# Performance work log

Hardware: AMD Instinct MI355X
Metric: run time of the kernel (lower is better)

The kernel has to match this reference:

```python
import jax, jax.numpy as jnp
import numpy as np


def setup_inputs() -> dict:
    key = jax.random.key(0)
    k1, k2, k3 = jax.random.split(key, 3)
    B, S, E = 4, 4096, 512
    x = jax.random.normal(k1, (B, S, E), dtype=jnp.float32)
    # xavier_uniform for Linear weights; zero biases (per _reset_parameters)
    lim_qkv = float(np.sqrt(6.0 / (E + 3 * E)))
    W_qkv = jax.random.uniform(k2, (3 * E, E), minval=-lim_qkv, maxval=lim_qkv, dtype=jnp.float32)
    b_qkv = jnp.zeros((3 * E,), dtype=jnp.float32)
    lim_out = float(np.sqrt(6.0 / (E + E)))
    W_out = jax.random.uniform(k3, (E, E), minval=-lim_out, maxval=lim_out, dtype=jnp.float32)
    b_out = jnp.zeros((E,), dtype=jnp.float32)
    return {"x": x, "W_qkv": W_qkv, "b_qkv": b_qkv, "W_out": W_out, "b_out": b_out}


def reference(x, W_qkv, b_qkv, W_out, b_out):
    B, S, E = x.shape
    H = 8
    D = E // H
    qkv = x @ W_qkv.T + b_qkv                      # [B,S,3E]
    qkv = qkv.reshape(B, S, H, 3 * D)
    q, k, v = jnp.split(qkv, 3, axis=-1)            # each [B,S,H,D]
    q = jax.nn.sigmoid(q)
    k = jax.nn.sigmoid(k)
    # flow conservation normalizers (sum over seq dim=1, then feature dim=3)
    i = jnp.sum(q * jnp.sum(k, axis=1, keepdims=True), axis=3, keepdims=True)      # [B,S,H,1]
    o = jnp.sum(k * jnp.sum(q, axis=1, keepdims=True), axis=3, keepdims=True)
    i_hat = jnp.sum(q * jnp.sum(k / o, axis=1, keepdims=True), axis=3, keepdims=True)
    o_hat = jnp.sum(k * jnp.sum(q / i, axis=1, keepdims=True), axis=3, keepdims=True)
    # NOTE: faithful to source — matmul batches over (B,S) and contracts the HEAD axis
    vw = v * jax.nn.softmax(o_hat, axis=1)          # [B,S,H,D]
    kv = jnp.einsum('bshd,bshe->bsde', k, vw)       # [B,S,D,D]
    r = jnp.einsum('bshd,bsde->bshe', q / i, kv) * jax.nn.sigmoid(i_hat)  # [B,S,H,D]
    values = r.reshape(B, S, E)
    return values @ W_out.T + b_out
```

## Files before the change

### kernel.cpp

```cpp
#include <hip/hip_runtime.h>
#include <cstdint>
#include <cstddef>

#define B_ 4
#define S_ 4096
#define E_ 512
#define NPOS 16384
#define QKVC 1536
#define K_ 512

typedef unsigned short u16;
typedef u16    u16x8  __attribute__((ext_vector_type(8)));
typedef u16    u16x4  __attribute__((ext_vector_type(4)));
typedef __bf16 bf16x8 __attribute__((ext_vector_type(8)));
typedef float  f32x4  __attribute__((ext_vector_type(4)));

__device__ __forceinline__ u16 f2bf(float f) {
    unsigned u = __builtin_bit_cast(unsigned, f);
    unsigned r = (u + 0x7fffu + ((u >> 16) & 1u)) >> 16;
    return (u16)r;
}
__device__ __forceinline__ float bf2f(u16 u) {
    return __builtin_bit_cast(float, (unsigned)u << 16);
}
__device__ __forceinline__ float rcpf(float x) { return __builtin_amdgcn_rcpf(x); }

__device__ __forceinline__ void async16(const void* g, void* lds) {
    __builtin_amdgcn_global_load_lds(
        (const __attribute__((address_space(1))) unsigned int*)g,
        (__attribute__((address_space(3))) unsigned int*)lds, 16, 0, 0);
}

__global__ void cvt_kernel(const float4* __restrict__ in, u16x4* __restrict__ out, int n4) {
    int i = blockIdx.x * 256 + threadIdx.x;
    if (i < n4) {
        float4 v = in[i];
        u16x4 o;
        o[0] = f2bf(v.x); o[1] = f2bf(v.y); o[2] = f2bf(v.z); o[3] = f2bf(v.w);
        out[i] = o;
    }
}

__global__ __launch_bounds__(256) void gemm_qkv(
        const u16* __restrict__ A, const u16* __restrict__ Bw,
        const float* __restrict__ bias,
        u16* __restrict__ Qb, u16* __restrict__ Kb, u16* __restrict__ Vb,
        int K) {
    __shared__ u16 As[128 * 32];
    __shared__ u16 Bs[128 * 32];
    const int tid  = threadIdx.x;
    const int wave = tid >> 6, lane = tid & 63;
    const int m0 = blockIdx.y * 128, n0 = blockIdx.x * 128;
    const int wm = (wave & 1) * 64, wn = (wave >> 1) * 64;

    const int srow = wave * 16 + (lane >> 2);
    const int scol = (lane & 3) * 8;
    const u16* Ap = A  + (size_t)(m0 + srow) * K + scol;
    const u16* Bp = Bw + (size_t)(n0 + srow) * K + scol;
    u16* AsW = &As[wave * 512];
    u16* BsW = &Bs[wave * 512];
    const size_t rstep = (size_t)64 * K;

    f32x4 acc[4][4] = {};
    const int fr = lane & 15, fk = (lane >> 4) * 8;

    for (int k0 = 0; k0 < K; k0 += 32) {
        async16(Ap + k0,         AsW);
        async16(Ap + k0 + rstep, AsW + 2048);
        async16(Bp + k0,         BsW);
        async16(Bp + k0 + rstep, BsW + 2048);
        __syncthreads();
        bf16x8 a[4], b[4];
        #pragma unroll
        for (int i = 0; i < 4; ++i)
            a[i] = *(const bf16x8*)&As[(wm + i * 16 + fr) * 32 + fk];
        #pragma unroll
        for (int j = 0; j < 4; ++j)
            b[j] = *(const bf16x8*)&Bs[(wn + j * 16 + fr) * 32 + fk];
        #pragma unroll
        for (int i = 0; i < 4; ++i)
            #pragma unroll
            for (int j = 0; j < 4; ++j)
                acc[i][j] = __builtin_amdgcn_mfma_f32_16x16x32_bf16(a[i], b[j], acc[i][j], 0, 0, 0);
        __syncthreads();
    }

    const int cn = lane & 15, rb = (lane >> 4) * 4;
    const int cg   = (n0 + wn) >> 6;
    const int type = cg % 3;
    const int hb   = cg / 3;
    u16* dst = (type == 0) ? Qb : (type == 1) ? Kb : Vb;
    const bool sg = (type < 2);
    #pragma unroll
    for (int i = 0; i < 4; ++i) {
        int mbase = m0 + wm + i * 16 + rb;
        #pragma unroll
        for (int j = 0; j < 4; ++j) {
            int ccol = j * 16 + cn;
            float bv = bias[n0 + wn + ccol];
            int outcol = hb * 64 + ccol;
            f32x4 av = acc[i][j];
            #pragma unroll
            for (int r = 0; r < 4; ++r) {
                float v = av[r] + bv;
                if (sg) v = 1.f / (1.f + __expf(-v));
                dst[(size_t)(mbase + r) * 512 + outcol] = f2bf(v);
            }
        }
    }
}

__global__ __launch_bounds__(256) void gemm_out(
        const u16* __restrict__ A, const u16* __restrict__ Bw,
        const float* __restrict__ bias, float* __restrict__ C,
        int N, int K) {
    __shared__ u16 As[128 * 32];
    __shared__ u16 Bs[128 * 32];
    const int tid  = threadIdx.x;
    const int wave = tid >> 6, lane = tid & 63;
    const int m0 = blockIdx.y * 128, n0 = blockIdx.x * 128;
    const int wm = (wave & 1) * 64, wn = (wave >> 1) * 64;
    const int srow = wave * 16 + (lane >> 2);
    const int scol = (lane & 3) * 8;
    const u16* Ap = A  + (size_t)(m0 + srow) * K + scol;
    const u16* Bp = Bw + (size_t)(n0 + srow) * K + scol;
    u16* AsW = &As[wave * 512];
    u16* BsW = &Bs[wave * 512];
    const size_t rstep = (size_t)64 * K;
    f32x4 acc[4][4] = {};
    const int fr = lane & 15, fk = (lane >> 4) * 8;
    for (int k0 = 0; k0 < K; k0 += 32) {
        async16(Ap + k0,         AsW);
        async16(Ap + k0 + rstep, AsW + 2048);
        async16(Bp + k0,         BsW);
        async16(Bp + k0 + rstep, BsW + 2048);
        __syncthreads();
        bf16x8 a[4], b[4];
        #pragma unroll
        for (int i = 0; i < 4; ++i)
            a[i] = *(const bf16x8*)&As[(wm + i * 16 + fr) * 32 + fk];
        #pragma unroll
        for (int j = 0; j < 4; ++j)
            b[j] = *(const bf16x8*)&Bs[(wn + j * 16 + fr) * 32 + fk];
        #pragma unroll
        for (int i = 0; i < 4; ++i)
            #pragma unroll
            for (int j = 0; j < 4; ++j)
                acc[i][j] = __builtin_amdgcn_mfma_f32_16x16x32_bf16(a[i], b[j], acc[i][j], 0, 0, 0);
        __syncthreads();
    }
    const int cn = lane & 15, rb = (lane >> 4) * 4;
    #pragma unroll
    for (int i = 0; i < 4; ++i) {
        int mbase = m0 + wm + i * 16 + rb;
        #pragma unroll
        for (int j = 0; j < 4; ++j) {
            int nn = n0 + wn + j * 16 + cn;
            float bv = bias[nn];
            f32x4 av = acc[i][j];
            #pragma unroll
            for (int r = 0; r < 4; ++r)
                C[(size_t)(mbase + r) * N + nn] = av[r] + bv;
        }
    }
}

__global__ __launch_bounds__(256) void sum_qk(const u16* __restrict__ Qg, const u16* __restrict__ Kg,
                                              float* __restrict__ sumq, float* __restrict__ sumk) {
    int b = blockIdx.x, sc = blockIdx.y;
    int w = threadIdx.x >> 6, lane = threadIdx.x & 63;
    float aq[8] = {}, ak[8] = {};
    int p0 = b * S_ + sc * 32 + w * 8;
    for (int it = 0; it < 8; ++it) {
        size_t off = (size_t)(p0 + it) * 512 + lane * 8;
        u16x8 q8 = *(const u16x8*)(Qg + off);
        u16x8 k8 = *(const u16x8*)(Kg + off);
        #pragma unroll
        for (int j = 0; j < 8; ++j) { aq[j] += bf2f(q8[j]); ak[j] += bf2f(k8[j]); }
    }
    __shared__ float red[4][1024];
    #pragma unroll
    for (int j = 0; j < 8; ++j) {
        red[w][lane * 8 + j]       = aq[j];
        red[w][512 + lane * 8 + j] = ak[j];
    }
    __syncthreads();
    int t = threadIdx.x;
    #pragma unroll
    for (int rr = 0; rr < 4; ++rr) {
        int slot = rr * 256 + t;
        float s = red[0][slot] + red[1][slot] + red[2][slot] + red[3][slot];
        float* dst = (slot < 512) ? &sumq[b * 512 + slot] : &sumk[b * 512 + (slot - 512)];
        atomicAdd(dst, s);
    }
}

__global__ __launch_bounds__(256) void fused_io(const u16* __restrict__ Qg, const u16* __restrict__ Kg,
                                                const float* __restrict__ sumq, const float* __restrict__ sumk,
                                                float* __restrict__ iv,
                                                float* __restrict__ sumqi, float* __restrict__ sumko) {
    int b = blockIdx.x, sc = blockIdx.y;
    int w = threadIdx.x >> 6, lane = threadIdx.x & 63;
    float skL[8], sqL[8];
    #pragma unroll
    for (int j = 0; j < 8; ++j) {
        skL[j] = sumk[b * 512 + lane * 8 + j];
        sqL[j] = sumq[b * 512 + lane * 8 + j];
    }
    float aqi[8] = {}, ako[8] = {};
    int p0 = b * S_ + sc * 32 + w * 8;
    for (int it = 0; it < 8; ++it) {
        int p = p0 + it;
        size_t off = (size_t)p * 512 + lane * 8;
        u16x8 q8 = *(const u16x8*)(Qg + off);
        u16x8 k8 = *(const u16x8*)(Kg + off);
        float qf[8], kf[8];
        #pragma unroll
        for (int j = 0; j < 8; ++j) { qf[j] = bf2f(q8[j]); kf[j] = bf2f(k8[j]); }
        float di = 0.f, dox = 0.f;
        #pragma unroll
        for (int j = 0; j < 8; ++j) { di += qf[j] * skL[j]; dox += kf[j] * sqL[j]; }
        di  += __shfl_xor(di, 1);  di  += __shfl_xor(di, 2);  di  += __shfl_xor(di, 4);
        dox += __shfl_xor(dox, 1); dox += __shfl_xor(dox, 2); dox += __shfl_xor(dox, 4);
        if ((lane & 7) == 0) iv[(size_t)p * 8 + (lane >> 3)] = di;
        float ri = rcpf(di), ro = rcpf(dox);
        #pragma unroll
        for (int j = 0; j < 8; ++j) { aqi[j] += qf[j] * ri; ako[j] += kf[j] * ro; }
    }
    __shared__ float red[4][1024];
    #pragma unroll
    for (int j = 0; j < 8; ++j) {
        red[w][lane * 8 + j]       = aqi[j];
        red[w][512 + lane * 8 + j] = ako[j];
    }
    __syncthreads();
    int t = threadIdx.x;
    #pragma unroll
    for (int rr = 0; rr < 4; ++rr) {
        int slot = rr * 256 + t;
        float s = red[0][slot] + red[1][slot] + red[2][slot] + red[3][slot];
        float* dst = (slot < 512) ? &sumqi[b * 512 + slot] : &sumko[b * 512 + (slot - 512)];
        atomicAdd(dst, s);
    }
}

__global__ __launch_bounds__(256) void io2_kernel(const u16* __restrict__ Qg, const u16* __restrict__ Kg,
                                                  const float* __restrict__ sumqi, const float* __restrict__ sumko,
                                                  const float* __restrict__ iv,
                                                  float* __restrict__ rowsc, float* __restrict__ wexp,
                                                  float* __restrict__ sm) {
    int b = blockIdx.x, sc = blockIdx.y;
    int w = threadIdx.x >> 6, lane = threadIdx.x & 63;
    float skoL[8], sqiL[8];
    #pragma unroll
    for (int j = 0; j < 8; ++j) {
        skoL[j] = sumko[b * 512 + lane * 8 + j];
        sqiL[j] = sumqi[b * 512 + lane * 8 + j];
    }
    float smacc = 0.f;
    int p0 = b * S_ + sc * 32 + w * 8;
    for (int it = 0; it < 8; ++it) {
        int p = p0 + it;
        size_t off = (size_t)p * 512 + lane * 8;
        u16x8 q8 = *(const u16x8*)(Qg + off);
        u16x8 k8 = *(const u16x8*)(Kg + off);
        float dih = 0.f, doh = 0.f;
        #pragma unroll
        for (int j = 0; j < 8; ++j) {
            dih += bf2f(q8[j]) * skoL[j];
            doh += bf2f(k8[j]) * sqiL[j];
        }
        dih += __shfl_xor(dih, 1); dih += __shfl_xor(dih, 2); dih += __shfl_xor(dih, 4);
        doh += __shfl_xor(doh, 1); doh += __shfl_xor(doh, 2); doh += __shfl_xor(doh, 4);
        if ((lane & 7) == 0) {
            int h = lane >> 3;
            float sig = 1.f / (1.f + __expf(-dih));
            rowsc[(size_t)p * 8 + h] = sig * rcpf(iv[(size_t)p * 8 + h]);
            float we = __expf(fminf(doh, 80.f));
            wexp[(size_t)p * 8 + h] = we;
            smacc += we;
        }
    }
    __shared__ float sr[4][8];
    if ((lane & 7) == 0) sr[w][lane >> 3] = smacc;
    __syncthreads();
    if (threadIdx.x < 8)
        atomicAdd(&sm[b * 8 + threadIdx.x],
                  sr[0][threadIdx.x] + sr[1][threadIdx.x] + sr[2][threadIdx.x] + sr[3][threadIdx.x]);
}

__global__ __launch_bounds__(256) void finalize_kernel(
        const u16* __restrict__ Qg, const u16* __restrict__ Kg, const u16* __restrict__ Vg,
        const float* __restrict__ rowsc, const float* __restrict__ wexp, const float* __restrict__ sm,
        u16* __restrict__ Rg) {
    __shared__ float Ml[4][2][8][9];
    __shared__ float vw[4][2][8][68];
    int w = threadIdx.x >> 6, lane = threadIdx.x & 63;
    int p0 = (blockIdx.x * 4 + w) * 2;
    int b = p0 >> 12;

    {
        int pl = (lane >> 3) & 1, hh = lane & 7, quad = lane >> 4;
        const u16* qa = Qg + (size_t)(p0 + pl) * 512 + hh * 64 + quad * 8;
        const u16* ka = Kg + (size_t)(p0 + pl) * 512 + hh * 64 + quad * 8;
        bf16x8 a0 = __builtin_bit_cast(bf16x8, *(const u16x8*)qa);
        bf16x8 a1 = __builtin_bit_cast(bf16x8, *(const u16x8*)(qa + 32));
        bf16x8 b0 = __builtin_bit_cast(bf16x8, *(const u16x8*)ka);
        bf16x8 b1 = __builtin_bit_cast(bf16x8, *(const u16x8*)(ka + 32));
        f32x4 accm = {0.f, 0.f, 0.f, 0.f};
        accm = __builtin_amdgcn_mfma_f32_16x16x32_bf16(a0, b0, accm, 0, 0, 0);
        accm = __builtin_amdgcn_mfma_f32_16x16x32_bf16(a1, b1, accm, 0, 0, 0);
        if (((lane >> 5) & 1) == ((lane >> 3) & 1)) {
            int plm = lane >> 5, hr = ((lane >> 4) & 1) * 4, h2 = lane & 7;
            #pragma unroll
            for (int r = 0; r < 4; ++r) Ml[w][plm][hr + r][h2] = accm[r];
        }
    }
    {
        int hv = lane >> 3, e0 = (lane & 7) * 8;
        float invsm = rcpf(sm[b * 8 + hv]);
        #pragma unroll
        for (int pl = 0; pl < 2; ++pl) {
            u16x8 v8 = *(const u16x8*)(Vg + (size_t)(p0 + pl) * 512 + lane * 8);
            float wgt = wexp[(size_t)(p0 + pl) * 8 + hv] * invsm;
            f32x4 x0, x1;
            #pragma unroll
            for (int j = 0; j < 4; ++j) { x0[j] = bf2f(v8[j]) * wgt; x1[j] = bf2f(v8[4 + j]) * wgt; }
            *(f32x4*)&vw[w][pl][hv][e0]     = x0;
            *(f32x4*)&vw[w][pl][hv][e0 + 4] = x1;
        }
    }
    __syncthreads();
    {
        int pl = lane >> 5, idx = lane & 31, h = idx >> 2, eq = (idx & 3) * 16;
        float out[16] = {};
        #pragma unroll
        for (int h2 = 0; h2 < 8; ++h2) {
            float m = Ml[w][pl][h][h2];
            #pragma unroll
            for (int c = 0; c < 4; ++c) {
                f32x4 vv = *(const f32x4*)&vw[w][pl][h2][eq + c * 4];
                #pragma unroll
                for (int j = 0; j < 4; ++j) out[c * 4 + j] += m * vv[j];
            }
        }
        float rs = rowsc[(size_t)(p0 + pl) * 8 + h];
        u16x8 o0, o1;
        #pragma unroll
        for (int j = 0; j < 8; ++j) { o0[j] = f2bf(out[j] * rs); o1[j] = f2bf(out[8 + j] * rs); }
        u16* dst = Rg + (size_t)(p0 + pl) * 512 + h * 64 + eq;
        *(u16x8*)dst       = o0;
        *(u16x8*)(dst + 8) = o1;
    }
}

extern "C" void kernel_launch(void* const* d_in, const int* in_sizes, int n_in,
                              void* d_out, int out_size, void* d_ws, size_t ws_size,
                              hipStream_t stream) {
    const float* x    = (const float*)d_in[0];
    const float* Wqkv = (const float*)d_in[1];
    const float* bqkv = (const float*)d_in[2];
    const float* Wout = (const float*)d_in[3];
    const float* bout = (const float*)d_in[4];
    float* out = (float*)d_out;
    char* ws = (char*)d_ws;

    constexpr size_t SZ_XBF  = (size_t)NPOS * E_ * 2;
    constexpr size_t SZ_WQBF = (size_t)QKVC * E_ * 2;
    constexpr size_t SZ_WOBF = (size_t)E_ * E_ * 2;
    constexpr size_t SZ_QKVB = (size_t)NPOS * E_ * 2;
    constexpr size_t SZ_SUM  = (size_t)B_ * 512 * 4;
    constexpr size_t SZ_V8   = (size_t)NPOS * 8 * 4;

    size_t off = 0;
    u16*   xbf   = (u16*)(ws + off);   off += SZ_XBF;
    u16*   wqbf  = (u16*)(ws + off);   off += SZ_WQBF;
    u16*   wobf  = (u16*)(ws + off);   off += SZ_WOBF;
    u16*   Qb    = (u16*)(ws + off);   off += SZ_QKVB;
    u16*   Kb    = (u16*)(ws + off);   off += SZ_QKVB;
    u16*   Vb    = (u16*)(ws + off);   off += SZ_QKVB;
    char*  zbase = ws + off;
    float* sumq  = (float*)(ws + off); off += SZ_SUM;
    float* sumk  = (float*)(ws + off); off += SZ_SUM;
    float* sumqi = (float*)(ws + off); off += SZ_SUM;
    float* sumko = (float*)(ws + off); off += SZ_SUM;
    float* sm    = (float*)(ws + off); off += 256;
    size_t zlen  = (char*)(ws + off) - zbase;
    float* iv    = (float*)(ws + off); off += SZ_V8;
    float* rowsc = (float*)(ws + off); off += SZ_V8;
    float* wexp  = (float*)(ws + off); off += SZ_V8;
    u16*   rbf   = xbf;

    hipMemsetAsync(zbase, 0, zlen, stream);

    cvt_kernel<<<(NPOS * E_ / 4) / 256, 256, 0, stream>>>((const float4*)x, (u16x4*)xbf, NPOS * E_ / 4);
    cvt_kernel<<<(QKVC * E_ / 4) / 256, 256, 0, stream>>>((const float4*)Wqkv, (u16x4*)wqbf, QKVC * E_ / 4);
    cvt_kernel<<<(E_ * E_ / 4) / 256, 256, 0, stream>>>((const float4*)Wout, (u16x4*)wobf, E_ * E_ / 4);

    gemm_qkv<<<dim3(QKVC / 128, NPOS / 128), 256, 0, stream>>>(xbf, wqbf, bqkv, Qb, Kb, Vb, K_);

    sum_qk<<<dim3(B_, 128), 256, 0, stream>>>(Qb, Kb, sumq, sumk);
    fused_io<<<dim3(B_, 128), 256, 0, stream>>>(Qb, Kb, sumq, sumk, iv, sumqi, sumko);
    io2_kernel<<<dim3(B_, 128), 256, 0, stream>>>(Qb, Kb, sumqi, sumko, iv, rowsc, wexp, sm);
    finalize_kernel<<<NPOS / 8, 256, 0, stream>>>(Qb, Kb, Vb, rowsc, wexp, sm, rbf);

    gemm_out<<<dim3(E_ / 128, NPOS / 128), 256, 0, stream>>>(rbf, wobf, bout, out, E_, K_);
}
```

Baseline: 199.3 us.

## Fuse middle normalizer stages into persistent kernel with grid barriers

Merges the three fp32-to-bf16 conversion launches into one. Column sums of sigmoid Q/K now come from the QKV GEMM epilogue through atomics, which drops the separate sum pass. The io, io2 and finalize kernels become one 512-block kernel that keeps per-row intermediates in shared memory and uses two software grid barriers. This removes launch gaps and the global round-trips for iv, rowsc and wexp. It relies on all 512 blocks being co-resident, otherwise the grid barriers deadlock, and it adds atomic contention in the GEMM epilogue.

```diff
diff --git a/kernel.cpp b/kernel.cpp
--- a/kernel.cpp
+++ b/kernel.cpp
@@ -8,6 +8,7 @@
 #define NPOS 16384
 #define QKVC 1536
 #define K_ 512
+#define MIDBLK 512
 
 typedef unsigned short u16;
 typedef u16    u16x8  __attribute__((ext_vector_type(8)));
@@ -31,20 +32,37 @@
         (__attribute__((address_space(3))) unsigned int*)lds, 16, 0, 0);
 }
 
-__global__ void cvt_kernel(const float4* __restrict__ in, u16x4* __restrict__ out, int n4) {
+__device__ __forceinline__ void gbar(unsigned* ctr) {
+    __syncthreads();
+    if (threadIdx.x == 0) {
+        __hip_atomic_fetch_add(ctr, 1u, __ATOMIC_RELEASE, __HIP_MEMORY_SCOPE_AGENT);
+        while (__hip_atomic_load(ctr, __ATOMIC_ACQUIRE, __HIP_MEMORY_SCOPE_AGENT) < (unsigned)MIDBLK)
+            __builtin_amdgcn_s_sleep(2);
+    }
+    __syncthreads();
+}
+
+__global__ __launch_bounds__(256) void cvt3(
+        const float4* __restrict__ x, const float4* __restrict__ wq, const float4* __restrict__ wo,
+        u16x4* __restrict__ ox, u16x4* __restrict__ owq, u16x4* __restrict__ owo) {
+    const int n1 = NPOS * E_ / 4, n2 = QKVC * E_ / 4, n3 = E_ * E_ / 4;
     int i = blockIdx.x * 256 + threadIdx.x;
-    if (i < n4) {
-        float4 v = in[i];
-        u16x4 o;
-        o[0] = f2bf(v.x); o[1] = f2bf(v.y); o[2] = f2bf(v.z); o[3] = f2bf(v.w);
-        out[i] = o;
-    }
+    const float4* in; u16x4* out; int j;
+    if (i < n1)            { in = x;  out = ox;  j = i; }
+    else if (i < n1 + n2)  { in = wq; out = owq; j = i - n1; }
+    else if (i < n1+n2+n3) { in = wo; out = owo; j = i - n1 - n2; }
+    else return;
+    float4 v = in[j];
+    u16x4 o;
+    o[0] = f2bf(v.x); o[1] = f2bf(v.y); o[2] = f2bf(v.z); o[3] = f2bf(v.w);
+    out[j] = o;
 }
 
 __global__ __launch_bounds__(256) void gemm_qkv(
         const u16* __restrict__ A, const u16* __restrict__ Bw,
         const float* __restrict__ bias,
         u16* __restrict__ Qb, u16* __restrict__ Kb, u16* __restrict__ Vb,
+        float* __restrict__ sumq, float* __restrict__ sumk,
         int K) {
     __shared__ u16 As[128 * 32];
     __shared__ u16 Bs[128 * 32];
@@ -89,23 +107,32 @@
     const int cg   = (n0 + wn) >> 6;
     const int type = cg % 3;
     const int hb   = cg / 3;
+    const int bb   = m0 >> 12;
     u16* dst = (type == 0) ? Qb : (type == 1) ? Kb : Vb;
+    float* ssum = (type == 0) ? sumq : sumk;
     const bool sg = (type < 2);
     #pragma unroll
-    for (int i = 0; i < 4; ++i) {
-        int mbase = m0 + wm + i * 16 + rb;
-        #pragma unroll
-        for (int j = 0; j < 4; ++j) {
-            int ccol = j * 16 + cn;
-            float bv = bias[n0 + wn + ccol];
-            int outcol = hb * 64 + ccol;
+    for (int j = 0; j < 4; ++j) {
+        int ccol = j * 16 + cn;
+        float bv = bias[n0 + wn + ccol];
+        int outcol = hb * 64 + ccol;
+        float csum = 0.f;
+        #pragma unroll
+        for (int i = 0; i < 4; ++i) {
+            int mbase = m0 + wm + i * 16 + rb;
             f32x4 av = acc[i][j];
             #pragma unroll
             for (int r = 0; r < 4; ++r) {
                 float v = av[r] + bv;
                 if (sg) v = 1.f / (1.f + __expf(-v));
+                csum += v;
                 dst[(size_t)(mbase + r) * 512 + outcol] = f2bf(v);
             }
+        }
+        if (sg) {
+            csum += __shfl_xor(csum, 16);
+            csum += __shfl_xor(csum, 32);
+            if (lane < 16) atomicAdd(&ssum[bb * 512 + outcol], csum);
         }
     }
 }
@@ -165,192 +192,162 @@
     }
 }
 
-__global__ __launch_bounds__(256) void sum_qk(const u16* __restrict__ Qg, const u16* __restrict__ Kg,
-                                              float* __restrict__ sumq, float* __restrict__ sumk) {
-    int b = blockIdx.x, sc = blockIdx.y;
-    int w = threadIdx.x >> 6, lane = threadIdx.x & 63;
-    float aq[8] = {}, ak[8] = {};
-    int p0 = b * S_ + sc * 32 + w * 8;
-    for (int it = 0; it < 8; ++it) {
-        size_t off = (size_t)(p0 + it) * 512 + lane * 8;
-        u16x8 q8 = *(const u16x8*)(Qg + off);
-        u16x8 k8 = *(const u16x8*)(Kg + off);
-        #pragma unroll
-        for (int j = 0; j < 8; ++j) { aq[j] += bf2f(q8[j]); ak[j] += bf2f(k8[j]); }
-    }
+__global__ __launch_bounds__(256) void mid_kernel(
+        const u16* __restrict__ Qg, const u16* __restrict__ Kg, const u16* __restrict__ Vg,
+        const float* __restrict__ sumq, const float* __restrict__ sumk,
+        float* __restrict__ sumqi, float* __restrict__ sumko, float* __restrict__ sm,
+        unsigned* __restrict__ bar0, unsigned* __restrict__ bar1,
+        u16* __restrict__ Rg) {
     __shared__ float red[4][1024];
-    #pragma unroll
-    for (int j = 0; j < 8; ++j) {
-        red[w][lane * 8 + j]       = aq[j];
-        red[w][512 + lane * 8 + j] = ak[j];
-    }
-    __syncthreads();
-    int t = threadIdx.x;
-    #pragma unroll
-    for (int rr = 0; rr < 4; ++rr) {
-        int slot = rr * 256 + t;
-        float s = red[0][slot] + red[1][slot] + red[2][slot] + red[3][slot];
-        float* dst = (slot < 512) ? &sumq[b * 512 + slot] : &sumk[b * 512 + (slot - 512)];
-        atomicAdd(dst, s);
-    }
-}
-
-__global__ __launch_bounds__(256) void fused_io(const u16* __restrict__ Qg, const u16* __restrict__ Kg,
-                                                const float* __restrict__ sumq, const float* __restrict__ sumk,
-                                                float* __restrict__ iv,
-                                                float* __restrict__ sumqi, float* __restrict__ sumko) {
-    int b = blockIdx.x, sc = blockIdx.y;
-    int w = threadIdx.x >> 6, lane = threadIdx.x & 63;
-    float skL[8], sqL[8];
-    #pragma unroll
-    for (int j = 0; j < 8; ++j) {
-        skL[j] = sumk[b * 512 + lane * 8 + j];
-        sqL[j] = sumq[b * 512 + lane * 8 + j];
-    }
-    float aqi[8] = {}, ako[8] = {};
-    int p0 = b * S_ + sc * 32 + w * 8;
-    for (int it = 0; it < 8; ++it) {
-        int p = p0 + it;
-        size_t off = (size_t)p * 512 + lane * 8;
-        u16x8 q8 = *(const u16x8*)(Qg + off);
-        u16x8 k8 = *(const u16x8*)(Kg + off);
-        float qf[8], kf[8];
-        #pragma unroll
-        for (int j = 0; j < 8; ++j) { qf[j] = bf2f(q8[j]); kf[j] = bf2f(k8[j]); }
-        float di = 0.f, dox = 0.f;
-        #pragma unroll
-        for (int j = 0; j < 8; ++j) { di += qf[j] * skL[j]; dox += kf[j] * sqL[j]; }
-        di  += __shfl_xor(di, 1);  di  += __shfl_xor(di, 2);  di  += __shfl_xor(di, 4);
-        dox += __shfl_xor(dox, 1); dox += __shfl_xor(dox, 2); dox += __shfl_xor(dox, 4);
-        if ((lane & 7) == 0) iv[(size_t)p * 8 + (lane >> 3)] = di;
-        float ri = rcpf(di), ro = rcpf(dox);
-        #pragma unroll
-        for (int j = 0; j < 8; ++j) { aqi[j] += qf[j] * ri; ako[j] += kf[j] * ro; }
-    }
-    __shared__ float red[4][1024];
-    #pragma unroll
-    for (int j = 0; j < 8; ++j) {
-        red[w][lane * 8 + j]       = aqi[j];
-        red[w][512 + lane * 8 + j] = ako[j];
-    }
-    __syncthreads();
-    int t = threadIdx.x;
-    #pragma unroll
-    for (int rr = 0; rr < 4; ++rr) {
-        int slot = rr * 256 + t;
-        float s = red[0][slot] + red[1][slot] + red[2][slot] + red[3][slot];
-        float* dst = (slot < 512) ? &sumqi[b * 512 + slot] : &sumko[b * 512 + (slot - 512)];
-        atomicAdd(dst, s);
-    }
-}
-
-__global__ __launch_bounds__(256) void io2_kernel(const u16* __restrict__ Qg, const u16* __restrict__ Kg,
-                                                  const float* __restrict__ sumqi, const float* __restrict__ sumko,
-                                                  const float* __restrict__ iv,
-                                                  float* __restrict__ rowsc, float* __restrict__ wexp,
-                                                  float* __restrict__ sm) {
-    int b = blockIdx.x, sc = blockIdx.y;
-    int w = threadIdx.x >> 6, lane = threadIdx.x & 63;
-    float skoL[8], sqiL[8];
-    #pragma unroll
-    for (int j = 0; j < 8; ++j) {
-        skoL[j] = sumko[b * 512 + lane * 8 + j];
-        sqiL[j] = sumqi[b * 512 + lane * 8 + j];
-    }
-    float smacc = 0.f;
-    int p0 = b * S_ + sc * 32 + w * 8;
-    for (int it = 0; it < 8; ++it) {
-        int p = p0 + it;
-        size_t off = (size_t)p * 512 + lane * 8;
-        u16x8 q8 = *(const u16x8*)(Qg + off);
-        u16x8 k8 = *(const u16x8*)(Kg + off);
-        float dih = 0.f, doh = 0.f;
-        #pragma unroll
-        for (int j = 0; j < 8; ++j) {
-            dih += bf2f(q8[j]) * skoL[j];
-            doh += bf2f(k8[j]) * sqiL[j];
-        }
-        dih += __shfl_xor(dih, 1); dih += __shfl_xor(dih, 2); dih += __shfl_xor(dih, 4);
-        doh += __shfl_xor(doh, 1); doh += __shfl_xor(doh, 2); doh += __shfl_xor(doh, 4);
-        if ((lane & 7) == 0) {
-            int h = lane >> 3;
-            float sig = 1.f / (1.f + __expf(-dih));
-            rowsc[(size_t)p * 8 + h] = sig * rcpf(iv[(size_t)p * 8 + h]);
-            float we = __expf(fminf(doh, 80.f));
-            wexp[(size_t)p * 8 + h] = we;
-            smacc += we;
-        }
-    }
-    __shared__ float sr[4][8];
-    if ((lane & 7) == 0) sr[w][lane >> 3] = smacc;
-    __syncthreads();
-    if (threadIdx.x < 8)
-        atomicAdd(&sm[b * 8 + threadIdx.x],
-                  sr[0][threadIdx.x] + sr[1][threadIdx.x] + sr[2][threadIdx.x] + sr[3][threadIdx.x]);
-}
-
-__global__ __launch_bounds__(256) void finalize_kernel(
-        const u16* __restrict__ Qg, const u16* __restrict__ Kg, const u16* __restrict__ Vg,
-        const float* __restrict__ rowsc, const float* __restrict__ wexp, const float* __restrict__ sm,
-        u16* __restrict__ Rg) {
+    __shared__ float ivs[32][8];
+    __shared__ float rsc[32][8];
+    __shared__ float wxp[32][8];
+    __shared__ float smr[4][8];
     __shared__ float Ml[4][2][8][9];
     __shared__ float vw[4][2][8][68];
-    int w = threadIdx.x >> 6, lane = threadIdx.x & 63;
-    int p0 = (blockIdx.x * 4 + w) * 2;
-    int b = p0 >> 12;
+
+    const int b = blockIdx.x >> 7, sc = blockIdx.x & 127;
+    const int pbase = b * S_ + sc * 32;
+    const int w = threadIdx.x >> 6, lane = threadIdx.x & 63;
+    const int tid = threadIdx.x;
+    const int p0 = pbase + w * 8;
 
     {
-        int pl = (lane >> 3) & 1, hh = lane & 7, quad = lane >> 4;
-        const u16* qa = Qg + (size_t)(p0 + pl) * 512 + hh * 64 + quad * 8;
-        const u16* ka = Kg + (size_t)(p0 + pl) * 512 + hh * 64 + quad * 8;
-        bf16x8 a0 = __builtin_bit_cast(bf16x8, *(const u16x8*)qa);
-        bf16x8 a1 = __builtin_bit_cast(bf16x8, *(const u16x8*)(qa + 32));
-        bf16x8 b0 = __builtin_bit_cast(bf16x8, *(const u16x8*)ka);
-        bf16x8 b1 = __builtin_bit_cast(bf16x8, *(const u16x8*)(ka + 32));
-        f32x4 accm = {0.f, 0.f, 0.f, 0.f};
-        accm = __builtin_amdgcn_mfma_f32_16x16x32_bf16(a0, b0, accm, 0, 0, 0);
-        accm = __builtin_amdgcn_mfma_f32_16x16x32_bf16(a1, b1, accm, 0, 0, 0);
-        if (((lane >> 5) & 1) == ((lane >> 3) & 1)) {
-            int plm = lane >> 5, hr = ((lane >> 4) & 1) * 4, h2 = lane & 7;
-            #pragma unroll
-            for (int r = 0; r < 4; ++r) Ml[w][plm][hr + r][h2] = accm[r];
-        }
-    }
+        float skL[8], sqL[8];
+        #pragma unroll
+        for (int j = 0; j < 8; ++j) {
+            skL[j] = sumk[b * 512 + lane * 8 + j];
+            sqL[j] = sumq[b * 512 + lane * 8 + j];
+        }
+        float aqi[8] = {}, ako[8] = {};
+        for (int it = 0; it < 8; ++it) {
+            int p = p0 + it;
+            size_t off = (size_t)p * 512 + lane * 8;
+            u16x8 q8 = *(const u16x8*)(Qg + off);
+            u16x8 k8 = *(const u16x8*)(Kg + off);
+            float qf[8], kf[8];
+            #pragma unroll
+            for (int j = 0; j < 8; ++j) { qf[j] = bf2f(q8[j]); kf[j] = bf2f(k8[j]); }
+            float di = 0.f, dox = 0.f;
+            #pragma unroll
+            for (int j = 0; j < 8; ++j) { di += qf[j] * skL[j]; dox += kf[j] * sqL[j]; }
+            di  += __shfl_xor(di, 1);  di  += __shfl_xor(di, 2);  di  += __shfl_xor(di, 4);
+            dox += __shfl_xor(dox, 1); dox += __shfl_xor(dox, 2); dox += __shfl_xor(dox, 4);
+            if ((lane & 7) == 0) ivs[w * 8 + it][lane >> 3] = di;
+            float ri = rcpf(di), ro = rcpf(dox);
+            #pragma unroll
+            for (int j = 0; j < 8; ++j) { aqi[j] += qf[j] * ri; ako[j] += kf[j] * ro; }
+        }
+        #pragma unroll
+        for (int j = 0; j < 8; ++j) {
+            red[w][lane * 8 + j]       = aqi[j];
+            red[w][512 + lane * 8 + j] = ako[j];
+        }
+        __syncthreads();
+        #pragma unroll
+        for (int rr = 0; rr < 4; ++rr) {
+            int slot = rr * 256 + tid;
+            float s = red[0][slot] + red[1][slot] + red[2][slot] + red[3][slot];
+            float* dstp = (slot < 512) ? &sumqi[b * 512 + slot] : &sumko[b * 512 + (slot - 512)];
+            atomicAdd(dstp, s);
+        }
+    }
+    gbar(bar0);
+
     {
-        int hv = lane >> 3, e0 = (lane & 7) * 8;
-        float invsm = rcpf(sm[b * 8 + hv]);
-        #pragma unroll
-        for (int pl = 0; pl < 2; ++pl) {
-            u16x8 v8 = *(const u16x8*)(Vg + (size_t)(p0 + pl) * 512 + lane * 8);
-            float wgt = wexp[(size_t)(p0 + pl) * 8 + hv] * invsm;
-            f32x4 x0, x1;
-            #pragma unroll
-            for (int j = 0; j < 4; ++j) { x0[j] = bf2f(v8[j]) * wgt; x1[j] = bf2f(v8[4 + j]) * wgt; }
-            *(f32x4*)&vw[w][pl][hv][e0]     = x0;
-            *(f32x4*)&vw[w][pl][hv][e0 + 4] = x1;
-        }
-    }
-    __syncthreads();
-    {
-        int pl = lane >> 5, idx = lane & 31, h = idx >> 2, eq = (idx & 3) * 16;
-        float out[16] = {};
-        #pragma unroll
-        for (int h2 = 0; h2 < 8; ++h2) {
-            float m = Ml[w][pl][h][h2];
-            #pragma unroll
-            for (int c = 0; c < 4; ++c) {
-                f32x4 vv = *(const f32x4*)&vw[w][pl][h2][eq + c * 4];
+        float skoL[8], sqiL[8];
+        #pragma unroll
+        for (int j = 0; j < 8; ++j) {
+            skoL[j] = sumko[b * 512 + lane * 8 + j];
+            sqiL[j] = sumqi[b * 512 + lane * 8 + j];
+        }
+        float smacc = 0.f;
+        for (int it = 0; it < 8; ++it) {
+            int p = p0 + it;
+            size_t off = (size_t)p * 512 + lane * 8;
+            u16x8 q8 = *(const u16x8*)(Qg + off);
+            u16x8 k8 = *(const u16x8*)(Kg + off);
+            float dih = 0.f, doh = 0.f;
+            #pragma unroll
+            for (int j = 0; j < 8; ++j) {
+                dih += bf2f(q8[j]) * skoL[j];
+                doh += bf2f(k8[j]) * sqiL[j];
+            }
+            dih += __shfl_xor(dih, 1); dih += __shfl_xor(dih, 2); dih += __shfl_xor(dih, 4);
+            doh += __shfl_xor(doh, 1); doh += __shfl_xor(doh, 2); doh += __shfl_xor(doh, 4);
+            if ((lane & 7) == 0) {
+                int pi = w * 8 + it, h = lane >> 3;
+                float sig = 1.f / (1.f + __expf(-dih));
+                rsc[pi][h] = sig * rcpf(ivs[pi][h]);
+                float we = __expf(fminf(doh, 80.f));
+                wxp[pi][h] = we;
+                smacc += we;
+            }
+        }
+        if ((lane & 7) == 0) smr[w][lane >> 3] = smacc;
+        __syncthreads();
+        if (tid < 8)
+            atomicAdd(&sm[b * 8 + tid], smr[0][tid] + smr[1][tid] + smr[2][tid] + smr[3][tid]);
+    }
+    gbar(bar1);
+
+    const float invsm = rcpf(sm[b * 8 + (lane >> 3)]);
+    for (int it2 = 0; it2 < 4; ++it2) {
+        int pl0 = w * 8 + it2 * 2;
+        int pp = pbase + pl0;
+        {
+            int pl = (lane >> 3) & 1, hh = lane & 7, quad = lane >> 4;
+            const u16* qa = Qg + (size_t)(pp + pl) * 512 + hh * 64 + quad * 8;
+            const u16* ka = Kg + (size_t)(pp + pl) * 512 + hh * 64 + quad * 8;
+            bf16x8 a0 = __builtin_bit_cast(bf16x8, *(const u16x8*)qa);
+            bf16x8 a1 = __builtin_bit_cast(bf16x8, *(const u16x8*)(qa + 32));
+            bf16x8 b0 = __builtin_bit_cast(bf16x8, *(const u16x8*)ka);
+            bf16x8 b1 = __builtin_bit_cast(bf16x8, *(const u16x8*)(ka + 32));
+            f32x4 accm = {0.f, 0.f, 0.f, 0.f};
+            accm = __builtin_amdgcn_mfma_f32_16x16x32_bf16(a0, b0, accm, 0, 0, 0);
+            accm = __builtin_amdgcn_mfma_f32_16x16x32_bf16(a1, b1, accm, 0, 0, 0);
+            if (((lane >> 5) & 1) == ((lane >> 3) & 1)) {
+                int plm = lane >> 5, hr = ((lane >> 4) & 1) * 4, h2 = lane & 7;
                 #pragma unroll
-                for (int j = 0; j < 4; ++j) out[c * 4 + j] += m * vv[j];
-            }
-        }
-        float rs = rowsc[(size_t)(p0 + pl) * 8 + h];
-        u16x8 o0, o1;
-        #pragma unroll
-        for (int j = 0; j < 8; ++j) { o0[j] = f2bf(out[j] * rs); o1[j] = f2bf(out[8 + j] * rs); }
-        u16* dst = Rg + (size_t)(p0 + pl) * 512 + h * 64 + eq;
-        *(u16x8*)dst       = o0;
-        *(u16x8*)(dst + 8) = o1;
+                for (int r = 0; r < 4; ++r)
+                    Ml[w][plm][hr + r][h2] = accm[r] * rsc[pl0 + plm][hr + r];
+            }
+        }
+        {
+            int hv = lane >> 3, e0 = (lane & 7) * 8;
+            #pragma unroll
+            for (int pl = 0; pl < 2; ++pl) {
+                u16x8 v8 = *(const u16x8*)(Vg + (size_t)(pp + pl) * 512 + lane * 8);
+                float wgt = wxp[pl0 + pl][hv] * invsm;
+                f32x4 x0, x1;
+                #pragma unroll
+                for (int j = 0; j < 4; ++j) { x0[j] = bf2f(v8[j]) * wgt; x1[j] = bf2f(v8[4 + j]) * wgt; }
+                *(f32x4*)&vw[w][pl][hv][e0]     = x0;
+                *(f32x4*)&vw[w][pl][hv][e0 + 4] = x1;
+            }
+        }
+        __syncthreads();
+        {
+            int pl = lane >> 5, idx = lane & 31, h = idx >> 2, eq = (idx & 3) * 16;
+            float outv[16] = {};
+            #pragma unroll
+            for (int h2 = 0; h2 < 8; ++h2) {
+                float m = Ml[w][pl][h][h2];
+                #pragma unroll
+                for (int c = 0; c < 4; ++c) {
+                    f32x4 vv = *(const f32x4*)&vw[w][pl][h2][eq + c * 4];
+                    #pragma unroll
+                    for (int j = 0; j < 4; ++j) outv[c * 4 + j] += m * vv[j];
+                }
+            }
+            u16x8 o0, o1;
+            #pragma unroll
+            for (int j = 0; j < 8; ++j) { o0[j] = f2bf(outv[j]); o1[j] = f2bf(outv[8 + j]); }
+            u16* dstp = Rg + (size_t)(pp + pl) * 512 + h * 64 + eq;
+            *(u16x8*)dstp       = o0;
+            *(u16x8*)(dstp + 8) = o1;
+        }
+        __syncthreads();
     }
 }
 
@@ -370,7 +367,6 @@
     constexpr size_t SZ_WOBF = (size_t)E_ * E_ * 2;
     constexpr size_t SZ_QKVB = (size_t)NPOS * E_ * 2;
     constexpr size_t SZ_SUM  = (size_t)B_ * 512 * 4;
-    constexpr size_t SZ_V8   = (size_t)NPOS * 8 * 4;
 
     size_t off = 0;
     u16*   xbf   = (u16*)(ws + off);   off += SZ_XBF;
@@ -385,24 +381,26 @@
     float* sumqi = (float*)(ws + off); off += SZ_SUM;
     float* sumko = (float*)(ws + off); off += SZ_SUM;
     float* sm    = (float*)(ws + off); off += 256;
+    unsigned* bar0 = (unsigned*)(ws + off); off += 128;
+    unsigned* bar1 = (unsigned*)(ws + off); off += 128;
     size_t zlen  = (char*)(ws + off) - zbase;
-    float* iv    = (float*)(ws + off); off += SZ_V8;
-    float* rowsc = (float*)(ws + off); off += SZ_V8;
-    float* wexp  = (float*)(ws + off); off += SZ_V8;
     u16*   rbf   = xbf;
 
     hipMemsetAsync(zbase, 0, zlen, stream);
 
-    cvt_kernel<<<(NPOS * E_ / 4) / 256, 256, 0, stream>>>((const float4*)x, (u16x4*)xbf, NPOS * E_ / 4);
-    cvt_kernel<<<(QKVC * E_ / 4) / 256, 256, 0, stream>>>((const float4*)Wqkv, (u16x4*)wqbf, QKVC * E_ / 4);
-    cvt_kernel<<<(E_ * E_ / 4) / 256, 256, 0, stream>>>((const float4*)Wout, (u16x4*)wobf, E_ * E_ / 4);
-
-    gemm_qkv<<<dim3(QKVC / 128, NPOS / 128), 256, 0, stream>>>(xbf, wqbf, bqkv, Qb, Kb, Vb, K_);
-
-    sum_qk<<<dim3(B_, 128), 256, 0, stream>>>(Qb, Kb, sumq, sumk);
-    fused_io<<<dim3(B_, 128), 256, 0, stream>>>(Qb, Kb, sumq, sumk, iv, sumqi, sumko);
-    io2_kernel<<<dim3(B_, 128), 256, 0, stream>>>(Qb, Kb, sumqi, sumko, iv, rowsc, wexp, sm);
-    finalize_kernel<<<NPOS / 8, 256, 0, stream>>>(Qb, Kb, Vb, rowsc, wexp, sm, rbf);
-
-    gemm_out<<<dim3(E_ / 128, NPOS / 128), 256, 0, stream>>>(rbf, wobf, bout, out, E_, K_);
-}
+    {
+        const int n4 = (NPOS * E_ + QKVC * E_ + E_ * E_) / 4;
+        cvt3<<<(n4 + 255) / 256, 256, 0, stream>>>(
+            (const float4*)x, (const float4*)Wqkv, (const float4*)Wout,
+            (u16x4*)xbf, (u16x4*)wqbf, (u16x4*)wobf);
+    }
+
+    gemm_qkv<<<dim3(QKVC / 128, NPOS / 128), 256, 0, stream>>>(
+        xbf, wqbf, bqkv, Qb, Kb, Vb, sumq, sumk, K_);
+
+    mid_kernel<<<MIDBLK, 256, 0, stream>>>(
+        Qb, Kb, Vb, sumq, sumk, sumqi, sumko, sm, bar0, bar1, rbf);
+
+    gemm_out<<<dim3(E_ / 128, NPOS / 128), 256, 0, stream>>>(
+        rbf, wobf, bout, out, E_, K_);
+}
```

Result: slower. 269.1 us (+35.0%).
